# Kernel tuning notes

Hardware: AMD Instinct MI355X
Metric: run time of the kernel (lower is better)

## Reference

```python
import jax, jax.numpy as jnp
import numpy as np

EPS = 1e-12  # torch F.normalize eps

def _l2norm(t):
    # normalize along last axis, clamp norm like torch.nn.functional.normalize
    n = jnp.sqrt(jnp.sum(t * t, axis=-1, keepdims=True))
    return t / jnp.maximum(n, EPS)

def setup_inputs() -> dict:
    key = jax.random.key(0)
    k1, k2, k3 = jax.random.split(key, 3)
    B, N, C, h = 4, 16384, 512, 8
    x = jax.random.normal(k1, (B, N, C), dtype=jnp.float32)
    qkv_w = jax.random.normal(k2, (C, 3 * C), dtype=jnp.float32) * 0.02
    proj_w = jax.random.normal(k3, (C, C), dtype=jnp.float32) * 0.02
    proj_b = jnp.zeros((C,), dtype=jnp.float32)
    temperature = jnp.ones((h, 1, 1), dtype=jnp.float32)  # temperature_init=1.0
    return {"x": x, "H": 128, "W": 128, "qkv_w": qkv_w,
            "proj_w": proj_w, "proj_b": proj_b, "temperature": temperature}

def reference(x, H, W, qkv_w, proj_w, proj_b, temperature):
    B, N, C = x.shape
    h = temperature.shape[0]
    d = C // h
    qkv = (x @ qkv_w).reshape(B, N, 3, h, d)          # [B,N,3,h,d]
    qkv = jnp.transpose(qkv, (2, 0, 3, 1, 4))         # [3,B,h,N,d]
    q, k, v = qkv[0], qkv[1], qkv[2]
    # channel attention: transpose to [B,h,d,N], normalize over tokens
    q = _l2norm(jnp.swapaxes(q, -2, -1))              # [B,h,d,N]
    k = _l2norm(jnp.swapaxes(k, -2, -1))              # [B,h,d,N]
    v = jnp.swapaxes(v, -2, -1)                       # [B,h,d,N]
    attn = jnp.einsum('bhdn,bhen->bhde', q, k) * temperature  # [B,h,d,d]
    attn = jax.nn.softmax(attn, axis=-1)
    out = jnp.einsum('bhde,bhen->bhdn', attn, v)      # [B,h,d,N]
    out = jnp.transpose(out, (0, 3, 1, 2)).reshape(B, N, C)
    return out @ proj_w + proj_b
```

## Files before the change

### kernel.cpp

```cpp
#include <hip/hip_runtime.h>
#include <stdint.h>
#include <stddef.h>


typedef unsigned short u16;
typedef __attribute__((ext_vector_type(8))) unsigned short u16x8;
typedef __attribute__((ext_vector_type(8))) __bf16 bf16x8;
typedef __attribute__((ext_vector_type(4))) float f32x4;

#define B_DIM 4
#define N_TOK 16384
#define C_DIM 512
#define CQ3   1536
#define NROWS 65536

__constant__ int PTI[10] = {0, 0, 0, 0, 1, 1, 1, 2, 2, 3};
__constant__ int PTJ[10] = {0, 1, 2, 3, 1, 2, 3, 2, 3, 3};

__device__ __forceinline__ u16 f2bf(float f) {
  union { float f; uint32_t u; } v; v.f = f;
  uint32_t r = v.u + 0x7FFFu + ((v.u >> 16) & 1u);
  return (u16)(r >> 16);
}
__device__ __forceinline__ float bf2f(u16 u) {
  union { uint32_t u; float f; } v; v.u = ((uint32_t)u) << 16;
  return v.f;
}
__device__ __forceinline__ bf16x8 as_bf16x8(u16x8 u) {
  union { u16x8 u; bf16x8 b; } v; v.u = u; return v.b;
}
__device__ __forceinline__ bf16x8 ldfrag(const u16* p) {
  return as_bf16x8(*(const u16x8*)p);
}
__device__ __forceinline__ void gl_lds16(const void* g, void* l) {
  __builtin_amdgcn_global_load_lds(
      (const __attribute__((address_space(1))) uint32_t*)g,
      (__attribute__((address_space(3))) uint32_t*)l, 16, 0, 0);
}
#define VMDRAIN asm volatile("s_waitcnt vmcnt(0)" ::: "memory")

__global__ __launch_bounds__(256) void k_prep(const float* __restrict__ qkv_w,
                                              const float* __restrict__ proj_w,
                                              u16* __restrict__ wl,
                                              u16* __restrict__ pwl,
                                              u16* __restrict__ vA) {
  int g = blockIdx.x * 256 + threadIdx.x;
  if (g < 98304) {
    int c8 = g / CQ3, j = g - c8 * CQ3;
    u16x8 o;
#pragma unroll
    for (int i = 0; i < 8; ++i) o[i] = f2bf(qkv_w[(size_t)(c8 * 8 + i) * CQ3 + j]);
    *(u16x8*)(wl + (size_t)g * 8) = o;
  } else if (g < 131072) {
    int gg = g - 98304;
    int d8 = gg >> 9, j = gg & 511;
    u16x8 o;
#pragma unroll
    for (int i = 0; i < 8; ++i) o[i] = f2bf(proj_w[(size_t)(d8 * 8 + i) * 512 + j]);
    *(u16x8*)(pwl + (size_t)gg * 8) = o;
  } else {
    int gg = g - 131072;
    int c = gg >> 6, q = gg & 63;
    const float* s = qkv_w + (size_t)c * CQ3 + 1024 + q * 8;
    float4 v0 = *(const float4*)s, v1 = *(const float4*)(s + 4);
    u16x8 o;
    o[0] = f2bf(v0.x); o[1] = f2bf(v0.y); o[2] = f2bf(v0.z); o[3] = f2bf(v0.w);
    o[4] = f2bf(v1.x); o[5] = f2bf(v1.y); o[6] = f2bf(v1.z); o[7] = f2bf(v1.w);
    *(u16x8*)(vA + (size_t)gg * 8) = o;
  }
}

__global__ __launch_bounds__(256) void k_xc(const float* __restrict__ x,
                                            u16* __restrict__ xb,
                                            u16* __restrict__ xbT) {
  __shared__ __align__(16) u16 T[16384];
  const int bi = blockIdx.x;
  const int b = bi >> 9, tt = (bi >> 2) & 127, ct = bi & 3;
  const int n0 = tt * 128, c0 = ct * 128;
  const int tid = threadIdx.x;
  const int cb8 = (tid & 15) * 8;
  const int tch = tid >> 4;
  const float* src = x + (size_t)(b * N_TOK + n0 + tch * 8) * C_DIM + c0 + cb8;
  float v[8][8];
#pragma unroll
  for (int j = 0; j < 8; ++j) {
    float4 a0 = *(const float4*)(src + (size_t)j * C_DIM);
    float4 a1 = *(const float4*)(src + (size_t)j * C_DIM + 4);
    v[j][0] = a0.x; v[j][1] = a0.y; v[j][2] = a0.z; v[j][3] = a0.w;
    v[j][4] = a1.x; v[j][5] = a1.y; v[j][6] = a1.z; v[j][7] = a1.w;
  }
  u16* xbd = xb + (size_t)(b * N_TOK + n0 + tch * 8) * C_DIM + c0 + cb8;
#pragma unroll
  for (int j = 0; j < 8; ++j) {
    u16x8 o;
#pragma unroll
    for (int i = 0; i < 8; ++i) o[i] = f2bf(v[j][i]);
    *(u16x8*)(xbd + (size_t)j * C_DIM) = o;
  }
#pragma unroll
  for (int i = 0; i < 8; ++i) {
    int c_loc = cb8 + i;
    int pc = tch ^ (tid & 15);
    u16x8 o;
#pragma unroll
    for (int j = 0; j < 8; ++j) o[j] = f2bf(v[j][i]);
    *(u16x8*)&T[c_loc * 128 + pc * 8] = o;
  }
  __syncthreads();
#pragma unroll
  for (int t = 0; t < 8; ++t) {
    int c_loc = t * 16 + (tid >> 4);
    int lch = tid & 15;
    int pc = lch ^ ((c_loc >> 3) & 15);
    u16x8 o = *(const u16x8*)&T[c_loc * 128 + pc * 8];
    *(u16x8*)&xbT[(size_t)(b * C_DIM + c0 + c_loc) * N_TOK + n0 + lch * 8] = o;
  }
}

__global__ __launch_bounds__(256) void k_g(const u16* __restrict__ xbT, u16* __restrict__ Gp) {
  __shared__ __align__(16) u16 As[2][8192];
  __shared__ __align__(16) u16 Bs[2][8192];
  const int tid = threadIdx.x, lane = tid & 63, wid = tid >> 6;
  const int orig = blockIdx.x;
  const int wg = (orig & 7) * 80 + (orig >> 3);
  const int kc = wg / 40, rem = wg % 40;
  const int b = rem / 10, p = rem % 10;
  const int ti = PTI[p], tj = PTJ[p];
  const u16* abase = xbT + ((size_t)b * 512 + ti * 128) * N_TOK + kc * 1024;
  const u16* bbase = xbT + ((size_t)b * 512 + tj * 128) * N_TOK + kc * 1024;
  const int wr = wid >> 1, wc = wid & 1;

  auto stage = [&](int kb, int buf) {
#pragma unroll
    for (int s4 = 0; s4 < 4; ++s4) {
      int slot = s4 * 256 + tid;
      int idx = slot >> 3, kblk = slot & 7;
      int kcol = kb * 64 + ((kblk ^ (idx & 7)) * 8);
      gl_lds16(abase + (size_t)idx * N_TOK + kcol, &As[buf][slot * 8]);
      gl_lds16(bbase + (size_t)idx * N_TOK + kcol, &Bs[buf][slot * 8]);
    }
  };

  f32x4 acc[4][4];
#pragma unroll
  for (int i = 0; i < 4; ++i)
#pragma unroll
    for (int j = 0; j < 4; ++j) acc[i][j] = (f32x4){0.f, 0.f, 0.f, 0.f};

  stage(0, 0);
  VMDRAIN;
  __syncthreads();
  for (int kb = 0; kb < 16; ++kb) {
    const int cur = kb & 1;
    if (kb < 15) stage(kb + 1, cur ^ 1);
#pragma unroll
    for (int kk = 0; kk < 2; ++kk) {
      const int krow = kk * 4 + (lane >> 4);
      const int pk = krow ^ (lane & 7);
      bf16x8 af[4], bfr[4];
#pragma unroll
      for (int t = 0; t < 4; ++t)
        af[t] = *(const bf16x8*)&As[cur][((wr * 64 + t * 16 + (lane & 15)) * 8 + pk) * 8];
#pragma unroll
      for (int t = 0; t < 4; ++t)
        bfr[t] = *(const bf16x8*)&Bs[cur][((wc * 64 + t * 16 + (lane & 15)) * 8 + pk) * 8];
#pragma unroll
      for (int mt = 0; mt < 4; ++mt)
#pragma unroll
        for (int nt = 0; nt < 4; ++nt)
          acc[mt][nt] = __builtin_amdgcn_mfma_f32_16x16x32_bf16(af[mt], bfr[nt], acc[mt][nt], 0, 0, 0);
    }
    if (kb < 15) VMDRAIN;
    __syncthreads();
  }
  u16* wsl = &As[0][0] + wid * 4096;
#pragma unroll
  for (int mt = 0; mt < 4; ++mt)
#pragma unroll
    for (int nt = 0; nt < 4; ++nt)
#pragma unroll
      for (int r = 0; r < 4; ++r) {
        int row = mt * 16 + (lane >> 4) * 4 + r;
        int col = nt * 16 + (lane & 15);
        int slot = (col >> 3) ^ (row & 7);
        wsl[row * 64 + slot * 8 + (col & 7)] = f2bf(acc[mt][nt][r]);
      }
  u16* gdst = Gp + (size_t)(kc * 4 + b) * 262144;
#pragma unroll
  for (int it = 0; it < 8; ++it) {
    int rr = it * 8 + (lane >> 3);
    int slot = (lane & 7) ^ (rr & 7);
    *(u16x8*)&gdst[(size_t)(ti * 128 + wr * 64 + rr) * 512 + tj * 128 + wc * 64 + (lane & 7) * 8] =
        *(const u16x8*)&wsl[rr * 64 + slot * 8];
  }
}

__global__ __launch_bounds__(256) void k_red(const u16* __restrict__ Gp, u16* __restrict__ G) {
  const int bi = blockIdx.x;
  const int b = bi / 80, rem = bi % 80;
  const int p = rem >> 3, sl = rem & 7;
  const int ti = PTI[p], tj = PTJ[p];
  const int tid = threadIdx.x;
  const int row = sl * 16 + (tid >> 4);
  const int c0 = (tid & 15) * 8;
  const size_t off = (size_t)(ti * 128 + row) * 512 + tj * 128 + c0;
  float s[8];
#pragma unroll
  for (int i = 0; i < 8; ++i) s[i] = 0.f;
  const u16* src = Gp + (size_t)b * 262144 + off;
#pragma unroll 4
  for (int kc = 0; kc < 16; ++kc) {
    u16x8 v = *(const u16x8*)(src + (size_t)kc * 1048576);
#pragma unroll
    for (int i = 0; i < 8; ++i) s[i] += bf2f(v[i]);
  }
  u16x8 o;
#pragma unroll
  for (int i = 0; i < 8; ++i) o[i] = f2bf(s[i]);
  u16* gb = G + (size_t)b * 262144;
  *(u16x8*)(gb + off) = o;
  if (ti != tj) {
#pragma unroll
    for (int i = 0; i < 8; ++i)
      gb[(size_t)(tj * 128 + c0 + i) * 512 + ti * 128 + row] = o[i];
  }
}

__global__ __launch_bounds__(256) void k_gq(const u16* __restrict__ G,
                                            const u16* __restrict__ wl,
                                            u16* __restrict__ Gqk) {
  const int bi = blockIdx.x;
  const int b = bi >> 5, mt = (bi >> 3) & 3, nt2 = bi & 7;
  const int m0 = mt * 128, n0 = nt2 * 128;
  const int lane = threadIdx.x & 63, w = threadIdx.x >> 6;
  f32x4 acc[8][2];
#pragma unroll
  for (int i = 0; i < 8; ++i) { acc[i][0] = (f32x4){0,0,0,0}; acc[i][1] = (f32x4){0,0,0,0}; }
  for (int ks = 0; ks < 16; ++ks) {
    bf16x8 bfr[2];
#pragma unroll
    for (int nf = 0; nf < 2; ++nf)
      bfr[nf] = ldfrag(wl + ((size_t)(ks * 4 + (lane >> 4)) * CQ3 + n0 + w * 32 + nf * 16 + (lane & 15)) * 8);
#pragma unroll
    for (int mf = 0; mf < 8; ++mf) {
      bf16x8 af = ldfrag(G + (size_t)b * 262144 + (size_t)(m0 + mf * 16 + (lane & 15)) * 512 + ks * 32 + (lane >> 4) * 8);
#pragma unroll
      for (int nf = 0; nf < 2; ++nf)
        acc[mf][nf] = __builtin_amdgcn_mfma_f32_16x16x32_bf16(af, bfr[nf], acc[mf][nf], 0, 0, 0);
    }
  }
#pragma unroll
  for (int mf = 0; mf < 8; ++mf)
#pragma unroll
    for (int nf = 0; nf < 2; ++nf)
#pragma unroll
      for (int r = 0; r < 4; ++r) {
        int d = m0 + mf * 16 + (lane >> 4) * 4 + r;
        int j = n0 + w * 32 + nf * 16 + (lane & 15);
        Gqk[(size_t)b * 524288 + ((size_t)(d >> 3) * 1024 + j) * 8 + (d & 7)] = f2bf(acc[mf][nf][r]);
      }
}

__global__ __launch_bounds__(256) void k_s2(const u16* __restrict__ Gqk,
                                            const u16* __restrict__ wl,
                                            const u16* __restrict__ pwl,
                                            const float* __restrict__ temp,
                                            u16* __restrict__ Ml) {
  __shared__ float Ssh[4][4096];
  __shared__ u16 At[64 * 72];
  __shared__ float ssqsh[128];
  __shared__ float rqk[128];
  const int tid = threadIdx.x, lane = tid & 63, w = tid >> 6;
  const int bh = blockIdx.x, b = bh >> 3, hh = bh & 7;
  if (tid < 128) ssqsh[tid] = 0.f;

  f32x4 acc[4][4];
#pragma unroll
  for (int i = 0; i < 4; ++i)
#pragma unroll
    for (int j = 0; j < 4; ++j) acc[i][j] = (f32x4){0.f, 0.f, 0.f, 0.f};
  for (int ks = 0; ks < 4; ++ks) {
    const int crow = w * 16 + ks * 4 + (lane >> 4);
    bf16x8 aq[4], bk[4];
#pragma unroll
    for (int mf = 0; mf < 4; ++mf)
      aq[mf] = ldfrag(wl + ((size_t)crow * CQ3 + hh * 64 + mf * 16 + (lane & 15)) * 8);
#pragma unroll
    for (int nf = 0; nf < 4; ++nf)
      bk[nf] = ldfrag(Gqk + (size_t)b * 524288 + ((size_t)crow * 1024 + 512 + hh * 64 + nf * 16 + (lane & 15)) * 8);
#pragma unroll
    for (int mf = 0; mf < 4; ++mf)
#pragma unroll
      for (int nf = 0; nf < 4; ++nf)
        acc[mf][nf] = __builtin_amdgcn_mfma_f32_16x16x32_bf16(aq[mf], bk[nf], acc[mf][nf], 0, 0, 0);
  }
#pragma unroll
  for (int mf = 0; mf < 4; ++mf)
#pragma unroll
    for (int nf = 0; nf < 4; ++nf)
#pragma unroll
      for (int r = 0; r < 4; ++r)
        Ssh[w][(mf * 16 + (lane >> 4) * 4 + r) * 64 + nf * 16 + (lane & 15)] = acc[mf][nf][r];
  __syncthreads();
  for (int idx = tid; idx < 4096; idx += 256)
    Ssh[0][idx] = Ssh[0][idx] + Ssh[1][idx] + Ssh[2][idx] + Ssh[3][idx];

  {
    const int d = tid & 63, part = tid >> 6;
    float sq = 0.f, sk = 0.f;
    for (int co = 0; co < 16; ++co) {
      int c8 = part * 16 + co;
      u16x8 wq = *(const u16x8*)(wl + ((size_t)c8 * CQ3 + hh * 64 + d) * 8);
      u16x8 gq = *(const u16x8*)(Gqk + (size_t)b * 524288 + ((size_t)c8 * 1024 + hh * 64 + d) * 8);
      u16x8 wk = *(const u16x8*)(wl + ((size_t)c8 * CQ3 + 512 + hh * 64 + d) * 8);
      u16x8 gk = *(const u16x8*)(Gqk + (size_t)b * 524288 + ((size_t)c8 * 1024 + 512 + hh * 64 + d) * 8);
#pragma unroll
      for (int i = 0; i < 8; ++i) {
        sq += bf2f(wq[i]) * bf2f(gq[i]);
        sk += bf2f(wk[i]) * bf2f(gk[i]);
      }
    }
    atomicAdd(&ssqsh[d], sq);
    atomicAdd(&ssqsh[64 + d], sk);
  }
  __syncthreads();
  if (tid < 128) rqk[tid] = 1.f / fmaxf(sqrtf(fmaxf(ssqsh[tid], 0.f)), 1e-12f);
  __syncthreads();

  {
    const float tp = temp[hh];
    const int d = tid >> 2, q4 = tid & 3;
    float vals[16];
    float mx = -3.0e38f;
    const float rqd = rqk[d];
#pragma unroll
    for (int i = 0; i < 16; ++i) {
      float v = Ssh[0][d * 64 + q4 * 16 + i] * rqd * rqk[64 + q4 * 16 + i] * tp;
      vals[i] = v; mx = fmaxf(mx, v);
    }
    mx = fmaxf(mx, __shfl_xor(mx, 1));
    mx = fmaxf(mx, __shfl_xor(mx, 2));
    float sum = 0.f;
#pragma unroll
    for (int i = 0; i < 16; ++i) { vals[i] = __expf(vals[i] - mx); sum += vals[i]; }
    sum += __shfl_xor(sum, 1);
    sum += __shfl_xor(sum, 2);
    const float inv = 1.f / sum;
#pragma unroll
    for (int i = 0; i < 16; ++i) At[(q4 * 16 + i) * 72 + d] = f2bf(vals[i] * inv);
  }
  __syncthreads();

  f32x4 acc2[4][8];
#pragma unroll
  for (int i = 0; i < 4; ++i)
#pragma unroll
    for (int j = 0; j < 8; ++j) acc2[i][j] = (f32x4){0.f, 0.f, 0.f, 0.f};
#pragma unroll
  for (int s = 0; s < 2; ++s) {
    bf16x8 af[4], bfr[8];
#pragma unroll
    for (int mf = 0; mf < 4; ++mf)
      af[mf] = *(const bf16x8*)&At[(mf * 16 + (lane & 15)) * 72 + s * 32 + (lane >> 4) * 8];
#pragma unroll
    for (int nf = 0; nf < 8; ++nf)
      bfr[nf] = ldfrag(pwl + ((size_t)(hh * 8 + s * 4 + (lane >> 4)) * 512 + w * 128 + nf * 16 + (lane & 15)) * 8);
#pragma unroll
    for (int mf = 0; mf < 4; ++mf)
#pragma unroll
      for (int nf = 0; nf < 8; ++nf)
        acc2[mf][nf] = __builtin_amdgcn_mfma_f32_16x16x32_bf16(af[mf], bfr[nf], acc2[mf][nf], 0, 0, 0);
  }
#pragma unroll
  for (int mf = 0; mf < 4; ++mf)
#pragma unroll
    for (int nf = 0; nf < 8; ++nf)
#pragma unroll
      for (int r = 0; r < 4; ++r) {
        int e = mf * 16 + (lane >> 4) * 4 + r;
        int j = w * 128 + nf * 16 + (lane & 15);
        int cc = hh * 64 + e;
        Ml[(size_t)b * 262144 + ((size_t)(cc >> 3) * 512 + j) * 8 + (cc & 7)] = f2bf(acc2[mf][nf][r]);
      }
}

__global__ __launch_bounds__(256) void k_p(const u16* __restrict__ vA,
                                           const u16* __restrict__ Ml,
                                           u16* __restrict__ Pl,
                                           const u16* __restrict__ xb) {
  const int bi = blockIdx.x;
  if (bi >= 64) {
    const float4* p = (const float4*)xb;
    float sx = 0.f, sy = 0.f, sz = 0.f, sw = 0.f;
    for (size_t i = (size_t)(bi - 64) * 256 + threadIdx.x; i < 4194304;
         i += (size_t)1984 * 256) {
      float4 v = p[i];
      sx += v.x; sy += v.y; sz += v.z; sw += v.w;
    }
    asm volatile("" :: "v"(sx), "v"(sy), "v"(sz), "v"(sw));
    return;
  }
  const int b = bi >> 4, ct = (bi >> 2) & 3, jt = bi & 3;
  const int m0 = ct * 128, j0 = jt * 128;
  const int lane = threadIdx.x & 63, w = threadIdx.x >> 6;
  f32x4 acc[8][2];
#pragma unroll
  for (int i = 0; i < 8; ++i) { acc[i][0] = (f32x4){0,0,0,0}; acc[i][1] = (f32x4){0,0,0,0}; }
  for (int ks = 0; ks < 16; ++ks) {
    bf16x8 bfr[2];
#pragma unroll
    for (int nf = 0; nf < 2; ++nf)
      bfr[nf] = ldfrag(Ml + (size_t)b * 262144 + ((size_t)(ks * 4 + (lane >> 4)) * 512 + j0 + w * 32 + nf * 16 + (lane & 15)) * 8);
#pragma unroll
    for (int mf = 0; mf < 8; ++mf) {
      bf16x8 af = ldfrag(vA + (size_t)(m0 + mf * 16 + (lane & 15)) * 512 + ks * 32 + (lane >> 4) * 8);
#pragma unroll
      for (int nf = 0; nf < 2; ++nf)
        acc[mf][nf] = __builtin_amdgcn_mfma_f32_16x16x32_bf16(af, bfr[nf], acc[mf][nf], 0, 0, 0);
    }
  }
#pragma unroll
  for (int mf = 0; mf < 8; ++mf)
#pragma unroll
    for (int nf = 0; nf < 2; ++nf)
#pragma unroll
      for (int r = 0; r < 4; ++r) {
        int c = m0 + mf * 16 + (lane >> 4) * 4 + r;
        int j = j0 + w * 32 + nf * 16 + (lane & 15);
        Pl[(size_t)b * 262144 + ((size_t)(c >> 3) * 512 + j) * 8 + (c & 7)] = f2bf(acc[mf][nf][r]);
      }
}

__global__ __launch_bounds__(256, 4) void k_out(const u16* __restrict__ xb,
                                                const u16* __restrict__ Pl,
                                                const float* __restrict__ pb,
                                                float* __restrict__ out) {
  __shared__ __align__(16) u16 As[8192];
  __shared__ __align__(16) u16 Bs[8192];
  const int tid = threadIdx.x;
  const int orig = blockIdx.x;
  const int wg = (orig & 7) * 256 + (orig >> 3);
  const int cb = wg & 3, rb = wg >> 2;
  const int row0 = rb * 128, col0 = cb * 128;
  const int b = rb >> 7;
  const int lane = tid & 63, wid = tid >> 6;
  const int wr = wid >> 1, wc = wid & 1;
  float bias[4];
#pragma unroll
  for (int nt = 0; nt < 4; ++nt) bias[nt] = pb[col0 + wc * 64 + nt * 16 + (lane & 15)];

  f32x4 acc[4][4];
#pragma unroll
  for (int i = 0; i < 4; ++i)
#pragma unroll
    for (int j = 0; j < 4; ++j) acc[i][j] = (f32x4){0.f, 0.f, 0.f, 0.f};

  const u16* pbase = Pl + (size_t)b * 262144;
  for (int kb = 0; kb < 8; ++kb) {
#pragma unroll
    for (int s4 = 0; s4 < 4; ++s4) {
      int slot = s4 * 256 + tid;
      int idx = slot >> 3, kblk = slot & 7;
      gl_lds16(xb + (size_t)(row0 + idx) * C_DIM + kb * 64 + ((kblk ^ (idx & 7)) * 8), &As[slot * 8]);
      int kblkB = slot >> 7, j = slot & 127;
      gl_lds16(pbase + ((size_t)(kb * 8 + kblkB) * 512 + col0 + j) * 8, &Bs[slot * 8]);
    }
    __syncthreads();
#pragma unroll
    for (int kk = 0; kk < 2; ++kk) {
      const int krow = kk * 4 + (lane >> 4);
      const int pk = krow ^ (lane & 7);
      bf16x8 af[4], bfr[4];
#pragma unroll
      for (int t = 0; t < 4; ++t)
        af[t] = *(const bf16x8*)&As[((wr * 64 + t * 16 + (lane & 15)) * 8 + pk) * 8];
#pragma unroll
      for (int t = 0; t < 4; ++t)
        bfr[t] = *(const bf16x8*)&Bs[(krow * 128 + wc * 64 + t * 16 + (lane & 15)) * 8];
#pragma unroll
      for (int mt = 0; mt < 4; ++mt)
#pragma unroll
        for (int nt = 0; nt < 4; ++nt)
          acc[mt][nt] = __builtin_amdgcn_mfma_f32_16x16x32_bf16(af[mt], bfr[nt], acc[mt][nt], 0, 0, 0);
    }
    __syncthreads();
  }
  float* slice = (wid < 2) ? (float*)&As[wid * 4096] : (float*)&Bs[(wid - 2) * 4096];
#pragma unroll
  for (int half = 0; half < 2; ++half) {
#pragma unroll
    for (int m2 = 0; m2 < 2; ++m2)
#pragma unroll
      for (int nt = 0; nt < 4; ++nt)
#pragma unroll
        for (int r = 0; r < 4; ++r) {
          int row = m2 * 16 + (lane >> 4) * 4 + r;
          int col = nt * 16 + (lane & 15);
          int slot = (col >> 2) ^ (row & 15);
          slice[row * 64 + slot * 4 + (col & 3)] = acc[half * 2 + m2][nt][r] + bias[nt];
        }
#pragma unroll
    for (int it = 0; it < 8; ++it) {
      int rr = it * 4 + (lane >> 4);
      int s = (lane & 15) ^ (rr & 15);
      *(float4*)&out[(size_t)(row0 + wr * 64 + half * 32 + rr) * C_DIM + col0 + wc * 64 + (lane & 15) * 4] =
          *(const float4*)&slice[rr * 64 + s * 4];
    }
  }
}

extern "C" void kernel_launch(void* const* d_in, const int* in_sizes, int n_in,
                              void* d_out, int out_size, void* d_ws, size_t ws_size,
                              hipStream_t stream) {
  const float* x      = (const float*)d_in[0];
  const float* qkv_w  = (const float*)d_in[3];
  const float* proj_w = (const float*)d_in[4];
  const float* proj_b = (const float*)d_in[5];
  const float* temp   = (const float*)d_in[6];
  float* out = (float*)d_out;

  char* ws = (char*)d_ws;
  u16* xb  = (u16*)(ws);
  u16* xbT = (u16*)(ws + 67108864);
  u16* wl  = (u16*)(ws + 134217728);
  u16* pwl = (u16*)(ws + 135790592);
  u16* vA  = (u16*)(ws + 136314880);
  u16* Gp  = (u16*)(ws + 136839168);
  u16* G   = (u16*)(ws + 170393600);
  u16* Gqk = (u16*)(ws + 172490752);
  u16* Ml  = (u16*)(ws + 176685056);
  u16* Pl  = (u16*)(ws + 178782208);

  k_xc<<<2048, 256, 0, stream>>>(x, xb, xbT);
  k_prep<<<640, 256, 0, stream>>>(qkv_w, proj_w, wl, pwl, vA);
  k_g<<<640, 256, 0, stream>>>(xbT, Gp);
  k_red<<<320, 256, 0, stream>>>(Gp, G);
  k_gq<<<128, 256, 0, stream>>>(G, wl, Gqk);
  k_s2<<<32, 256, 0, stream>>>(Gqk, wl, pwl, temp, Ml);
  k_p<<<2048, 256, 0, stream>>>(vA, Ml, Pl, xb);
  k_out<<<2048, 256, 0, stream>>>(xb, Pl, proj_b, out);
}
```

Measured before the change: 223.3 us.

## Double-buffer k_out LDS loads and move L2 prefetch blocks into k_gq

```diff
diff --git a/kernel.cpp b/kernel.cpp
--- a/kernel.cpp
+++ b/kernel.cpp
@@ -38,6 +38,7 @@
       (__attribute__((address_space(3))) uint32_t*)l, 16, 0, 0);
 }
 #define VMDRAIN asm volatile("s_waitcnt vmcnt(0)" ::: "memory")
+#define VM4     asm volatile("s_waitcnt vmcnt(4)" ::: "memory")
 
 __global__ __launch_bounds__(256) void k_prep(const float* __restrict__ qkv_w,
                                               const float* __restrict__ proj_w,
@@ -228,8 +229,20 @@
 
 __global__ __launch_bounds__(256) void k_gq(const u16* __restrict__ G,
                                             const u16* __restrict__ wl,
-                                            u16* __restrict__ Gqk) {
+                                            u16* __restrict__ Gqk,
+                                            const u16* __restrict__ xb) {
   const int bi = blockIdx.x;
+  if (bi >= 128) {
+    const float4* p = (const float4*)xb;
+    float sx = 0.f, sy = 0.f, sz = 0.f, sw = 0.f;
+    for (size_t i = (size_t)(bi - 128) * 256 + threadIdx.x; i < 4194304;
+         i += (size_t)1024 * 256) {
+      float4 v = p[i];
+      sx += v.x; sy += v.y; sz += v.z; sw += v.w;
+    }
+    asm volatile("" :: "v"(sx), "v"(sy), "v"(sz), "v"(sw));
+    return;
+  }
   const int b = bi >> 5, mt = (bi >> 3) & 3, nt2 = bi & 7;
   const int m0 = mt * 128, n0 = nt2 * 128;
   const int lane = threadIdx.x & 63, w = threadIdx.x >> 6;
@@ -386,20 +399,8 @@
 
 __global__ __launch_bounds__(256) void k_p(const u16* __restrict__ vA,
                                            const u16* __restrict__ Ml,
-                                           u16* __restrict__ Pl,
-                                           const u16* __restrict__ xb) {
+                                           u16* __restrict__ Pl) {
   const int bi = blockIdx.x;
-  if (bi >= 64) {
-    const float4* p = (const float4*)xb;
-    float sx = 0.f, sy = 0.f, sz = 0.f, sw = 0.f;
-    for (size_t i = (size_t)(bi - 64) * 256 + threadIdx.x; i < 4194304;
-         i += (size_t)1984 * 256) {
-      float4 v = p[i];
-      sx += v.x; sy += v.y; sz += v.z; sw += v.w;
-    }
-    asm volatile("" :: "v"(sx), "v"(sy), "v"(sz), "v"(sw));
-    return;
-  }
   const int b = bi >> 4, ct = (bi >> 2) & 3, jt = bi & 3;
   const int m0 = ct * 128, j0 = jt * 128;
   const int lane = threadIdx.x & 63, w = threadIdx.x >> 6;
@@ -435,8 +436,7 @@
                                                 const u16* __restrict__ Pl,
                                                 const float* __restrict__ pb,
                                                 float* __restrict__ out) {
-  __shared__ __align__(16) u16 As[8192];
-  __shared__ __align__(16) u16 Bs[8192];
+  __shared__ __align__(16) u16 L[16384];
   const int tid = threadIdx.x;
   const int orig = blockIdx.x;
   const int wg = (orig & 7) * 256 + (orig >> 3);
@@ -456,36 +456,55 @@
     for (int j = 0; j < 4; ++j) acc[i][j] = (f32x4){0.f, 0.f, 0.f, 0.f};
 
   const u16* pbase = Pl + (size_t)b * 262144;
-  for (int kb = 0; kb < 8; ++kb) {
-#pragma unroll
-    for (int s4 = 0; s4 < 4; ++s4) {
-      int slot = s4 * 256 + tid;
-      int idx = slot >> 3, kblk = slot & 7;
-      gl_lds16(xb + (size_t)(row0 + idx) * C_DIM + kb * 64 + ((kblk ^ (idx & 7)) * 8), &As[slot * 8]);
-      int kblkB = slot >> 7, j = slot & 127;
-      gl_lds16(pbase + ((size_t)(kb * 8 + kblkB) * 512 + col0 + j) * 8, &Bs[slot * 8]);
-    }
-    __syncthreads();
-#pragma unroll
-    for (int kk = 0; kk < 2; ++kk) {
-      const int krow = kk * 4 + (lane >> 4);
-      const int pk = krow ^ (lane & 7);
-      bf16x8 af[4], bfr[4];
-#pragma unroll
-      for (int t = 0; t < 4; ++t)
-        af[t] = *(const bf16x8*)&As[((wr * 64 + t * 16 + (lane & 15)) * 8 + pk) * 8];
-#pragma unroll
-      for (int t = 0; t < 4; ++t)
-        bfr[t] = *(const bf16x8*)&Bs[(krow * 128 + wc * 64 + t * 16 + (lane & 15)) * 8];
-#pragma unroll
-      for (int mt = 0; mt < 4; ++mt)
-#pragma unroll
-        for (int nt = 0; nt < 4; ++nt)
-          acc[mt][nt] = __builtin_amdgcn_mfma_f32_16x16x32_bf16(af[mt], bfr[nt], acc[mt][nt], 0, 0, 0);
-    }
-    __syncthreads();
-  }
-  float* slice = (wid < 2) ? (float*)&As[wid * 4096] : (float*)&Bs[(wid - 2) * 4096];
+  auto stage = [&](int kb, int buf) {
+#pragma unroll
+    for (int h = 0; h < 2; ++h) {
+      int s = h * 256 + tid;
+      int idx = s >> 2, kblk = s & 3;
+      int pkc = kblk ^ ((idx >> 2) & 3);
+      gl_lds16(xb + (size_t)(row0 + idx) * C_DIM + kb * 32 + pkc * 8,
+               &L[buf * 4096 + s * 8]);
+    }
+#pragma unroll
+    for (int h = 0; h < 2; ++h) {
+      int s = h * 256 + tid;
+      int kblk = s >> 7, j = s & 127;
+      gl_lds16(pbase + ((size_t)(kb * 4 + kblk) * 512 + col0 + j) * 8,
+               &L[8192 + buf * 4096 + s * 8]);
+    }
+  };
+
+  stage(0, 0);
+  VMDRAIN;
+  __builtin_amdgcn_s_barrier();
+  for (int kb = 0; kb < 16; ++kb) {
+    const int cur = kb & 1;
+    if (kb < 15) {
+      stage(kb + 1, cur ^ 1);
+      VM4;
+    } else {
+      VMDRAIN;
+    }
+    __builtin_amdgcn_s_barrier();
+    const int krow = lane >> 4;
+    const int pk = krow ^ ((lane >> 2) & 3);
+    bf16x8 af[4], bfr[4];
+#pragma unroll
+    for (int t = 0; t < 4; ++t)
+      af[t] = *(const bf16x8*)&L[cur * 4096 + ((wr * 64 + t * 16 + (lane & 15)) * 4 + pk) * 8];
+#pragma unroll
+    for (int t = 0; t < 4; ++t)
+      bfr[t] = *(const bf16x8*)&L[8192 + cur * 4096 + (krow * 128 + wc * 64 + t * 16 + (lane & 15)) * 8];
+    __builtin_amdgcn_s_setprio(1);
+#pragma unroll
+    for (int mt = 0; mt < 4; ++mt)
+#pragma unroll
+      for (int nt = 0; nt < 4; ++nt)
+        acc[mt][nt] = __builtin_amdgcn_mfma_f32_16x16x32_bf16(af[mt], bfr[nt], acc[mt][nt], 0, 0, 0);
+    __builtin_amdgcn_s_setprio(0);
+    __builtin_amdgcn_s_barrier();
+  }
+  float* slice = (float*)&L[wid * 4096];
 #pragma unroll
   for (int half = 0; half < 2; ++half) {
 #pragma unroll
@@ -535,8 +554,8 @@
   k_prep<<<640, 256, 0, stream>>>(qkv_w, proj_w, wl, pwl, vA);
   k_g<<<640, 256, 0, stream>>>(xbT, Gp);
   k_red<<<320, 256, 0, stream>>>(Gp, G);
-  k_gq<<<128, 256, 0, stream>>>(G, wl, Gqk);
+  k_gq<<<1152, 256, 0, stream>>>(G, wl, Gqk, xb);
   k_s2<<<32, 256, 0, stream>>>(Gqk, wl, pwl, temp, Ml);
-  k_p<<<2048, 256, 0, stream>>>(vA, Ml, Pl, xb);
+  k_p<<<64, 256, 0, stream>>>(vA, Ml, Pl);
   k_out<<<2048, 256, 0, stream>>>(xb, Pl, proj_b, out);
 }
```

Result: faster. 217.0 us (-2.8%).
